# Performance work log

Hardware: AMD Instinct MI355X
Metric: run time of the kernel (lower is better)

The kernel has to match this reference:

```python
import jax, jax.numpy as jnp
import numpy as np

NPOINT = 2048
NSAMPLE = 32
BN_EPS = 1e-5


def fps(xyz_t, npoint):
    """Furthest point sampling. xyz_t: [B,N,3] -> idx [B,npoint] (starts at index 0)."""
    B, N, _ = xyz_t.shape

    def step(carry, _):
        dist, last = carry  # dist [B,N], last [B]
        centroid = jnp.take_along_axis(xyz_t, last[:, None, None], axis=1)  # [B,1,3]
        d = jnp.sum((xyz_t - centroid) ** 2, axis=-1)  # [B,N]
        dist = jnp.minimum(dist, d)
        nxt = jnp.argmax(dist, axis=1).astype(jnp.int32)
        return (dist, nxt), last

    init = (jnp.full((B, N), 1e10, xyz_t.dtype), jnp.zeros((B,), jnp.int32))
    _, idx = jax.lax.scan(step, init, None, length=npoint)  # [npoint,B]
    return jnp.transpose(idx)  # [B,npoint]


def knn(k, query_t, ref_t):
    """query_t [B,S,3], ref_t [B,N,3] -> k-nearest indices [B,S,k]."""
    d = (jnp.sum(query_t ** 2, -1)[:, :, None]
         + jnp.sum(ref_t ** 2, -1)[:, None, :]
         - 2.0 * jnp.einsum('bsc,bnc->bsn', query_t, ref_t))  # [B,S,N]
    _, idx = jax.lax.top_k(-d, k)
    return idx


def group(feat_t, idx):
    """feat_t [B,N,C], idx [B,S,K] -> [B,S,K,C] gathered neighbors."""
    return jax.vmap(lambda f, i: f[i])(feat_t, idx)


def setup_inputs():
    key = jax.random.key(0)
    ks = jax.random.split(key, 8)
    B, N, C, D = 8, 8192, 3, 3
    mlp = [32, 32, 64]
    inp = {
        'xyz': jax.random.normal(ks[0], (B, C, N), jnp.float32),
        'points': jax.random.normal(ks[1], (B, D, N), jnp.float32),
    }
    last = D + 3  # conv input channels = in_channel + 3
    for i, oc in enumerate(mlp):
        inp[f'w{i}'] = jax.random.normal(ks[2 + i], (oc, last), jnp.float32) * (1.0 / np.sqrt(last))
        inp[f'g{i}'] = jnp.ones((oc,), jnp.float32)
        inp[f'b{i}'] = jnp.zeros((oc,), jnp.float32)
        last = oc
    return inp


def reference(xyz, points, w0, g0, b0, w1, g1, b1, w2, g2, b2):
    xyz_t = jnp.transpose(xyz, (0, 2, 1))        # [B,N,3]
    points_t = jnp.transpose(points, (0, 2, 1))  # [B,N,D]

    fps_idx = fps(xyz_t, NPOINT)                             # [B,S]
    new_xyz_t = jax.vmap(lambda f, i: f[i])(xyz_t, fps_idx)  # [B,S,3]

    knn_idx = knn(NSAMPLE, new_xyz_t, xyz_t)                 # [B,S,K]
    grouped_xyz = group(xyz_t, knn_idx)                      # [B,S,K,3]
    pos_diff = grouped_xyz - new_xyz_t[:, :, None, :]        # [B,S,K,3]
    grouped_pts = group(points_t, knn_idx)                   # [B,S,K,D]

    x = jnp.concatenate([pos_diff, grouped_pts], axis=-1)    # [B,S,K,3+D]
    for w, g, b in ((w0, g0, b0), (w1, g1, b1), (w2, g2, b2)):
        x = jnp.einsum('oc,bskc->bsko', w, x)                # 1x1 conv, no bias
        mean = jnp.mean(x, axis=(0, 1, 2))                   # BatchNorm2d (training stats)
        var = jnp.var(x, axis=(0, 1, 2))
        x = jax.nn.relu(g * (x - mean) * jax.lax.rsqrt(var + BN_EPS) + b)

    new_points = jnp.max(x, axis=2)  # max over K neighbors -> [B,S,C']
    new_xyz = jnp.transpose(new_xyz_t, (0, 2, 1))      # [B,3,S]
    new_points = jnp.transpose(new_points, (0, 2, 1))  # [B,C',S]
    return (new_xyz, new_points, fps_idx)
```

## Files before the change

kernel.cpp:

```cpp
#include <hip/hip_runtime.h>
#include <hip/hip_bf16.h>
#include <math.h>


#define NB 8
#define NN 8192
#define NS 2048
#define NK 32

__global__ __launch_bounds__(256) void prep_kernel(const float* __restrict__ xyz,
                                                   const float* __restrict__ pts,
                                                   float4* __restrict__ xyz4,
                                                   float4* __restrict__ pts4,
                                                   float* __restrict__ stats_acc,
                                                   int* __restrict__ prog) {
  int tid = threadIdx.x;
  if (blockIdx.x == 0) {
    stats_acc[tid] = 0.f;
    if (tid < 8) prog[tid] = 0;
  }
  int g = blockIdx.x * 256 + tid;
  int b = g >> 13, n = g & 8191;
  const float* xb = xyz + b * 3 * NN;
  float x = xb[n], y = xb[NN + n], z = xb[2 * NN + n];
  xyz4[g] = make_float4(x, y, z, fmaf(x, x, fmaf(y, y, z * z)));
  const float* pb = pts + b * 3 * NN;
  pts4[g] = make_float4(pb[n], pb[NN + n], pb[2 * NN + n], 0.f);
}

template <int CTRL>
__device__ __forceinline__ float dpp_max(float v) {
  int o = __builtin_amdgcn_update_dpp(__float_as_int(v), __float_as_int(v),
                                      CTRL, 0xf, 0xf, false);
  return fmaxf(v, __int_as_float(o));
}

__device__ __forceinline__ void insert32(float (&a)[32], float f) {
#pragma unroll
  for (int i = 31; i >= 1; --i) a[i] = fminf(a[i], fmaxf(a[i - 1], f));
  a[0] = fminf(a[0], f);
}

union MegaShm {
  struct {
    float lxyz[3 * NN];
    unsigned long long wslot[2][8];
  } f;
  float lbuf[256][33];
};

__global__ __launch_bounds__(512, 1) void mega_kernel(
    const float4* __restrict__ xyz4, const float4* __restrict__ pts4,
    float4* __restrict__ nxyz4, int* __restrict__ knn,
    const float* __restrict__ w0, float* __restrict__ stats_acc,
    int* __restrict__ prog, float* __restrict__ out_nxyz,
    float* __restrict__ out_fps) {
  __shared__ MegaShm sh;
  int tid = threadIdx.x;
  int lane = tid & 63, wid = tid >> 6;

  if (blockIdx.x < 8) {
    int b = blockIdx.x;
    const float4* xb = xyz4 + b * NN;

    for (int i = tid; i < NN; i += 512) {
      float4 t = xb[i];
      sh.f.lxyz[3 * i] = t.x;
      sh.f.lxyz[3 * i + 1] = t.y;
      sh.f.lxyz[3 * i + 2] = t.z;
    }
    float ax[16], ay[16], az[16], dist[16];
#pragma unroll
    for (int j = 0; j < 16; ++j) {
      float4 t = xb[(tid << 4) + j];
      asm volatile("v_accvgpr_write_b32 %0, %1" : "=a"(ax[j]) : "v"(t.x));
      asm volatile("v_accvgpr_write_b32 %0, %1" : "=a"(ay[j]) : "v"(t.y));
      asm volatile("v_accvgpr_write_b32 %0, %1" : "=a"(az[j]) : "v"(t.z));
      dist[j] = 1e10f;
    }
    float4 c0 = xb[0];
    float cx = c0.x, cy = c0.y, cz = c0.z;
    if (tid == 0) {
      nxyz4[b * NS] = c0;
      out_nxyz[b * 3 * NS] = c0.x;
      out_nxyz[b * 3 * NS + NS] = c0.y;
      out_nxyz[b * 3 * NS + 2 * NS] = c0.z;
      out_fps[b * NS] = 0.f;
    }
    __syncthreads();

    for (int s = 1; s < NS; ++s) {
#pragma unroll
      for (int j = 0; j < 16; ++j) {
        float x, y, z;
        asm volatile("v_accvgpr_read_b32 %0, %1" : "=v"(x) : "a"(ax[j]));
        asm volatile("v_accvgpr_read_b32 %0, %1" : "=v"(y) : "a"(ay[j]));
        asm volatile("v_accvgpr_read_b32 %0, %1" : "=v"(z) : "a"(az[j]));
        float dx = __fsub_rn(x, cx);
        float dy = __fsub_rn(y, cy);
        float dz = __fsub_rn(z, cz);
        float d = __fadd_rn(__fadd_rn(__fmul_rn(dx, dx), __fmul_rn(dy, dy)),
                            __fmul_rn(dz, dz));
        dist[j] = fminf(dist[j], d);
      }
      float lmax = dist[0];
#pragma unroll
      for (int j = 1; j < 16; ++j) lmax = fmaxf(lmax, dist[j]);

      float m = lmax;
      m = dpp_max<0x111>(m);
      m = dpp_max<0x112>(m);
      m = dpp_max<0x114>(m);
      m = dpp_max<0x118>(m);
      m = dpp_max<0x142>(m);
      m = dpp_max<0x143>(m);
      float wmax = __int_as_float(__builtin_amdgcn_readlane(__float_as_int(m), 63));

      unsigned long long bl = __ballot(lmax == wmax);
      int l0 = __ffsll(bl) - 1;
      int bj = 0;
      if (lmax == wmax) {
#pragma unroll
        for (int t = 15; t >= 0; --t)
          if (dist[t] == lmax) bj = t;
      }
      int gcand = (tid << 4) + bj;
      int gw = __builtin_amdgcn_readlane(gcand, l0);

      if (lane == 0)
        sh.f.wslot[s & 1][wid] =
            (((unsigned long long)__float_as_uint(wmax)) << 32) |
            (unsigned)(8191 - gw);
      __syncthreads();

      unsigned long long vm = sh.f.wslot[s & 1][0];
#pragma unroll
      for (int k = 1; k < 8; ++k) {
        unsigned long long o = sh.f.wslot[s & 1][k];
        vm = o > vm ? o : vm;
      }
      int gid = 8191 - (int)(unsigned)(vm & 0xFFFFFFFFull);
      gid = __builtin_amdgcn_readfirstlane(gid);

      cx = sh.f.lxyz[3 * gid];
      cy = sh.f.lxyz[3 * gid + 1];
      cz = sh.f.lxyz[3 * gid + 2];
      if (tid == 0) {
        float w = fmaf(cx, cx, fmaf(cy, cy, cz * cz));
        nxyz4[b * NS + s] = make_float4(cx, cy, cz, w);
        out_nxyz[b * 3 * NS + s] = cx;
        out_nxyz[b * 3 * NS + NS + s] = cy;
        out_nxyz[b * 3 * NS + 2 * NS + s] = cz;
        out_fps[b * NS + s] = (float)gid;
        if (((s + 1) & 63) == 0) {
          __threadfence();
          __hip_atomic_store(&prog[b], s + 1, __ATOMIC_RELEASE,
                             __HIP_MEMORY_SCOPE_AGENT);
        }
      }
    }
    return;
  }

  int w = blockIdx.x - 8;
  for (int ti = 0; ti < 2; ++ti) {
    if (ti == 1 && w >= 8) break;
    int tile_id = (ti == 0) ? w : 248 + w;
    int b = tile_id >> 5, tile = tile_id & 31;
    const float4* xb = xyz4 + b * NN;
    const float4* pb = pts4 + b * NN;

    if (tid == 0) {
      int need = (tile + 1) * 64;
      while (__hip_atomic_load(&prog[b], __ATOMIC_ACQUIRE,
                               __HIP_MEMORY_SCOPE_AGENT) < need)
        __builtin_amdgcn_s_sleep(64);
    }
    __syncthreads();

    float arr[32];
    if (tid < 256) {
      int q = tid & 63, chunk = tid >> 6;
      float4 Q = nxyz4[b * NS + tile * 64 + q];
      float qq = Q.w;
      float mx = -2.f * Q.x, my = -2.f * Q.y, mz = -2.f * Q.z;
#pragma unroll
      for (int i = 0; i < 32; ++i) arr[i] = __uint_as_float(0x7f7fffffu);
      const float4* refs = xb + chunk * 2048;
      int rbase = chunk * 2048;
      for (int r = 0; r < 2048; r += 4) {
        float4 R0 = refs[r], R1 = refs[r + 1], R2 = refs[r + 2], R3 = refs[r + 3];
        float d0 = fmaxf(fmaf(R0.x, mx, fmaf(R0.y, my, fmaf(R0.z, mz, R0.w + qq))), 0.f);
        float d1 = fmaxf(fmaf(R1.x, mx, fmaf(R1.y, my, fmaf(R1.z, mz, R1.w + qq))), 0.f);
        float d2 = fmaxf(fmaf(R2.x, mx, fmaf(R2.y, my, fmaf(R2.z, mz, R2.w + qq))), 0.f);
        float d3 = fmaxf(fmaf(R3.x, mx, fmaf(R3.y, my, fmaf(R3.z, mz, R3.w + qq))), 0.f);
        float f0 = __uint_as_float((__float_as_uint(d0) & 0xFFFFE000u) | (unsigned)(rbase + r));
        float f1 = __uint_as_float((__float_as_uint(d1) & 0xFFFFE000u) | (unsigned)(rbase + r + 1));
        float f2 = __uint_as_float((__float_as_uint(d2) & 0xFFFFE000u) | (unsigned)(rbase + r + 2));
        float f3 = __uint_as_float((__float_as_uint(d3) & 0xFFFFE000u) | (unsigned)(rbase + r + 3));
        if (f0 < arr[31]) insert32(arr, f0);
        if (f1 < arr[31]) insert32(arr, f1);
        if (f2 < arr[31]) insert32(arr, f2);
        if (f3 < arr[31]) insert32(arr, f3);
      }
#pragma unroll
      for (int i = 0; i < 32; ++i) sh.lbuf[tid][i] = arr[i];
    }
    __syncthreads();
    if (tid < 64) {
      for (int c = 1; c < 4; ++c)
        for (int i = 0; i < 32; ++i) {
          float f = sh.lbuf[c * 64 + tid][i];
          if (f < arr[31]) insert32(arr, f);
        }
      int base = (b * NS + tile * 64 + tid) * NK;
#pragma unroll
      for (int i = 0; i < 32; ++i) {
        knn[base + i] = (int)(__float_as_uint(arr[i]) & 0x1FFFu);
        sh.lbuf[tid][i] = arr[i];
      }
    }
    __syncthreads();

    float sum[32], sumsq[32];
#pragma unroll
    for (int o = 0; o < 32; ++o) { sum[o] = 0.f; sumsq[o] = 0.f; }
    for (int t = 0; t < 4; ++t) {
      int e = tid * 4 + t;
      int sq = e >> 5, k = e & 31;
      int nid = (int)(__float_as_uint(sh.lbuf[sq][k]) & 0x1FFFu);
      float4 Q = nxyz4[b * NS + tile * 64 + sq];
      float4 R = xb[nid];
      float4 P = pb[nid];
      float x0[6] = {R.x - Q.x, R.y - Q.y, R.z - Q.z, P.x, P.y, P.z};
#pragma unroll
      for (int o = 0; o < 32; ++o) {
        float a = w0[o * 6] * x0[0];
#pragma unroll
        for (int c = 1; c < 6; ++c) a = fmaf(w0[o * 6 + c], x0[c], a);
        sum[o] += a;
        sumsq[o] = fmaf(a, a, sumsq[o]);
      }
    }
#pragma unroll
    for (int o = 0; o < 32; ++o) {
      float s = sum[o], q = sumsq[o];
#pragma unroll
      for (int d = 1; d < 64; d <<= 1) { s += __shfl_xor(s, d); q += __shfl_xor(q, d); }
      sum[o] = s; sumsq[o] = q;
    }
    __syncthreads();
    float* cmb = &sh.lbuf[0][0];
    if (lane == 0) {
#pragma unroll
      for (int o = 0; o < 32; ++o) {
        cmb[wid * 64 + o] = sum[o];
        cmb[wid * 64 + 32 + o] = sumsq[o];
      }
    }
    __syncthreads();
    if (tid < 64) {
      float tot = 0.f;
#pragma unroll
      for (int wv = 0; wv < 8; ++wv) tot += cmb[wv * 64 + tid];
      atomicAdd(&stats_acc[tid], tot);
    }
    __syncthreads();
  }
}

template <int STAGE>
__global__ __launch_bounds__(256) void mlp_kernel(
    const float4* __restrict__ xyz4, const float4* __restrict__ pts4,
    const float4* __restrict__ nxyz4, const int* __restrict__ knn,
    const float* __restrict__ w0, const float* __restrict__ w1,
    const float* __restrict__ w2, const float* __restrict__ ab,
    float* __restrict__ acc, float* __restrict__ out_np) {
  constexpr int C = (STAGE == 2) ? 64 : 32;
  constexpr int SM = (STAGE == 3) ? 8 * 64 * 32 : 512;
  __shared__ float smem[SM];
  int blk = blockIdx.x;
  int b = blk >> 6, s0 = (blk & 63) * 32;
  int tid = threadIdx.x, sl = tid & 31, ksec = tid >> 5;
  int lane = tid & 63, wid = tid >> 6;
  int s = s0 + sl;
  float4 Q = nxyz4[b * NS + s];
  const float4* xb = xyz4 + b * NN;
  const float4* pb = pts4 + b * NN;
  const int* kb = knn + (b * NS + s) * NK + ksec * 4;

  float acc1[(STAGE == 3) ? 64 : C];
  float acc2[(STAGE == 3) ? 1 : C];
  if constexpr (STAGE == 3) {
#pragma unroll
    for (int o = 0; o < 64; ++o) acc1[o] = -3.4e38f;
  } else {
#pragma unroll
    for (int o = 0; o < C; ++o) { acc1[o] = 0.f; acc2[o] = 0.f; }
  }

  for (int kk = 0; kk < 4; ++kk) {
    int nid = kb[kk];
    float4 R = xb[nid];
    float4 P = pb[nid];
    float x0[6] = {R.x - Q.x, R.y - Q.y, R.z - Q.z, P.x, P.y, P.z};
    float h[32];
#pragma unroll
    for (int o = 0; o < 32; ++o) {
      float a = w0[o * 6] * x0[0];
#pragma unroll
      for (int c = 1; c < 6; ++c) a = fmaf(w0[o * 6 + c], x0[c], a);
      h[o] = fmaxf(fmaf(a, ab[o], ab[64 + o]), 0.f);
    }
    float h1[32];
#pragma unroll
    for (int o = 0; o < 32; ++o) {
      float a = 0.f;
#pragma unroll
      for (int i = 0; i < 32; ++i) a = fmaf(w1[o * 32 + i], h[i], a);
      h1[o] = a;
    }
    if constexpr (STAGE == 1) {
#pragma unroll
      for (int o = 0; o < 32; ++o) { acc1[o] += h1[o]; acc2[o] = fmaf(h1[o], h1[o], acc2[o]); }
    } else {
#pragma unroll
      for (int o = 0; o < 32; ++o) h1[o] = fmaxf(fmaf(h1[o], ab[128 + o], ab[192 + o]), 0.f);
#pragma unroll
      for (int o = 0; o < 64; ++o) {
        float a = 0.f;
#pragma unroll
        for (int i = 0; i < 32; ++i) a = fmaf(w2[o * 32 + i], h1[i], a);
        if constexpr (STAGE == 2) {
          acc1[o] += a;
          acc2[o] = fmaf(a, a, acc2[o]);
        } else {
          acc1[o] = fmaxf(acc1[o], fmaxf(fmaf(a, ab[256 + o], ab[320 + o]), 0.f));
        }
      }
    }
  }

  if constexpr (STAGE < 3) {
#pragma unroll
    for (int o = 0; o < C; ++o) {
      float v1 = acc1[o], v2 = acc2[o];
#pragma unroll
      for (int d = 1; d < 64; d <<= 1) { v1 += __shfl_xor(v1, d); v2 += __shfl_xor(v2, d); }
      acc1[o] = v1; acc2[o] = v2;
    }
    if (lane == 0) {
#pragma unroll
      for (int o = 0; o < C; ++o) {
        smem[wid * 2 * C + o] = acc1[o];
        smem[wid * 2 * C + C + o] = acc2[o];
      }
    }
    __syncthreads();
    if (tid < 2 * C) {
      float v = smem[tid] + smem[2 * C + tid] + smem[4 * C + tid] + smem[6 * C + tid];
      atomicAdd(&acc[tid], v);
    }
  } else {
#pragma unroll
    for (int o = 0; o < 64; ++o) smem[ksec * 2048 + o * 32 + sl] = acc1[o];
    __syncthreads();
#pragma unroll
    for (int i = 0; i < 8; ++i) {
      int e = i * 256 + tid;
      int ch = e >> 5, ss = e & 31;
      float v = smem[ch * 32 + ss];
#pragma unroll
      for (int ks = 1; ks < 8; ++ks) v = fmaxf(v, smem[ks * 2048 + ch * 32 + ss]);
      out_np[b * 64 * NS + ch * NS + s0 + ss] = v;
    }
  }
}

__global__ __launch_bounds__(64) void finalize_kernel(const float* __restrict__ acc,
                                                      const float* __restrict__ g,
                                                      const float* __restrict__ bt,
                                                      float* __restrict__ ab, int C) {
  int tid = threadIdx.x;
  if (tid < C) {
    float s1 = acc[tid];
    float s2 = acc[C + tid];
    const float ninv = 1.0f / 524288.0f;
    float mean = s1 * ninv;
    float var = s2 * ninv - mean * mean;
    float inv = 1.0f / sqrtf(var + 1e-5f);
    float a = g[tid] * inv;
    ab[tid] = a;
    ab[64 + tid] = bt[tid] - mean * a;
  }
}

extern "C" void kernel_launch(void* const* d_in, const int* in_sizes, int n_in,
                              void* d_out, int out_size, void* d_ws, size_t ws_size,
                              hipStream_t stream) {
  const float* xyz = (const float*)d_in[0];
  const float* pts = (const float*)d_in[1];
  const float* w0 = (const float*)d_in[2];
  const float* g0 = (const float*)d_in[3];
  const float* b0 = (const float*)d_in[4];
  const float* w1 = (const float*)d_in[5];
  const float* g1 = (const float*)d_in[6];
  const float* b1 = (const float*)d_in[7];
  const float* w2 = (const float*)d_in[8];
  const float* g2 = (const float*)d_in[9];
  const float* b2 = (const float*)d_in[10];
  float* out = (float*)d_out;
  float* ws = (float*)d_ws;

  float4* xyz4 = (float4*)ws;
  float4* pts4 = (float4*)(ws + 262144);
  float4* nxyz4 = (float4*)(ws + 524288);
  int* knn = (int*)(ws + 589824);
  float* stats_acc = ws + 1114112;
  int* prog = (int*)(ws + 1114368);
  float* ab = ws + 1114432;
  float* out_np = out + 49152;
  float* out_fps = out + 1097728;

  prep_kernel<<<256, 256, 0, stream>>>(xyz, pts, xyz4, pts4, stats_acc, prog);
  mega_kernel<<<256, 512, 0, stream>>>(xyz4, pts4, nxyz4, knn, w0, stats_acc,
                                       prog, out, out_fps);
  finalize_kernel<<<1, 64, 0, stream>>>(stats_acc, g0, b0, ab, 32);
  mlp_kernel<1><<<512, 256, 0, stream>>>(xyz4, pts4, nxyz4, knn, w0, w1, w2, ab,
                                         stats_acc + 64, nullptr);
  finalize_kernel<<<1, 64, 0, stream>>>(stats_acc + 64, g1, b1, ab + 128, 32);
  mlp_kernel<2><<<512, 256, 0, stream>>>(xyz4, pts4, nxyz4, knn, w0, w1, w2, ab,
                                         stats_acc + 128, nullptr);
  finalize_kernel<<<1, 64, 0, stream>>>(stats_acc + 128, g2, b2, ab + 256, 64);
  mlp_kernel<3><<<512, 256, 0, stream>>>(xyz4, pts4, nxyz4, knn, w0, w1, w2, ab,
                                         nullptr, out_np);
}
```

Measured before the change: 3.241 ms.

## Use packed FP32 math in FPS loop and batch centroid output writes

The furthest-point-sampling distance update now processes two points per instruction using v_pk_add_f32/v_pk_mul_f32, halving VALU instruction count in the serial loop. Per-step global stores of the selected centroid are replaced by a shared-memory ring of 64 entries, flushed cooperatively by 64 threads every 64 steps before the progress flag is published. This removes store latency from each serial iteration at the cost of two extra block barriers per 64 steps.

```diff
diff --git a/kernel.cpp b/kernel.cpp
--- a/kernel.cpp
+++ b/kernel.cpp
@@ -7,6 +7,15 @@
 #define NN 8192
 #define NS 2048
 #define NK 32
+
+typedef float v2f __attribute__((ext_vector_type(2)));
+
+__device__ __forceinline__ v2f pk_add(v2f a, v2f b) {
+  v2f d; asm("v_pk_add_f32 %0, %1, %2" : "=v"(d) : "v"(a), "v"(b)); return d;
+}
+__device__ __forceinline__ v2f pk_mul(v2f a, v2f b) {
+  v2f d; asm("v_pk_mul_f32 %0, %1, %2" : "=v"(d) : "v"(a), "v"(b)); return d;
+}
 
 __global__ __launch_bounds__(256) void prep_kernel(const float* __restrict__ xyz,
                                                    const float* __restrict__ pts,
@@ -45,6 +54,7 @@
   struct {
     float lxyz[3 * NN];
     unsigned long long wslot[2][8];
+    float4 cbuf[64];
   } f;
   float lbuf[256][33];
 };
@@ -80,28 +90,28 @@
     }
     float4 c0 = xb[0];
     float cx = c0.x, cy = c0.y, cz = c0.z;
-    if (tid == 0) {
-      nxyz4[b * NS] = c0;
-      out_nxyz[b * 3 * NS] = c0.x;
-      out_nxyz[b * 3 * NS + NS] = c0.y;
-      out_nxyz[b * 3 * NS + 2 * NS] = c0.z;
-      out_fps[b * NS] = 0.f;
-    }
+    if (tid == 0)
+      sh.f.cbuf[0] = make_float4(c0.x, c0.y, c0.z, 0.f);
     __syncthreads();
 
     for (int s = 1; s < NS; ++s) {
-#pragma unroll
-      for (int j = 0; j < 16; ++j) {
-        float x, y, z;
-        asm volatile("v_accvgpr_read_b32 %0, %1" : "=v"(x) : "a"(ax[j]));
-        asm volatile("v_accvgpr_read_b32 %0, %1" : "=v"(y) : "a"(ay[j]));
-        asm volatile("v_accvgpr_read_b32 %0, %1" : "=v"(z) : "a"(az[j]));
-        float dx = __fsub_rn(x, cx);
-        float dy = __fsub_rn(y, cy);
-        float dz = __fsub_rn(z, cz);
-        float d = __fadd_rn(__fadd_rn(__fmul_rn(dx, dx), __fmul_rn(dy, dy)),
-                            __fmul_rn(dz, dz));
-        dist[j] = fminf(dist[j], d);
+      v2f ncx = {-cx, -cx}, ncy = {-cy, -cy}, ncz = {-cz, -cz};
+#pragma unroll
+      for (int k = 0; k < 8; ++k) {
+        float x0, x1, y0, y1, z0, z1;
+        asm volatile("v_accvgpr_read_b32 %0, %1" : "=v"(x0) : "a"(ax[2 * k]));
+        asm volatile("v_accvgpr_read_b32 %0, %1" : "=v"(x1) : "a"(ax[2 * k + 1]));
+        asm volatile("v_accvgpr_read_b32 %0, %1" : "=v"(y0) : "a"(ay[2 * k]));
+        asm volatile("v_accvgpr_read_b32 %0, %1" : "=v"(y1) : "a"(ay[2 * k + 1]));
+        asm volatile("v_accvgpr_read_b32 %0, %1" : "=v"(z0) : "a"(az[2 * k]));
+        asm volatile("v_accvgpr_read_b32 %0, %1" : "=v"(z1) : "a"(az[2 * k + 1]));
+        v2f x01 = {x0, x1}, y01 = {y0, y1}, z01 = {z0, z1};
+        v2f dx = pk_add(x01, ncx);
+        v2f dy = pk_add(y01, ncy);
+        v2f dz = pk_add(z01, ncz);
+        v2f ss = pk_add(pk_add(pk_mul(dx, dx), pk_mul(dy, dy)), pk_mul(dz, dz));
+        dist[2 * k] = fminf(dist[2 * k], ss.x);
+        dist[2 * k + 1] = fminf(dist[2 * k + 1], ss.y);
       }
       float lmax = dist[0];
 #pragma unroll
@@ -145,14 +155,23 @@
       cx = sh.f.lxyz[3 * gid];
       cy = sh.f.lxyz[3 * gid + 1];
       cz = sh.f.lxyz[3 * gid + 2];
-      if (tid == 0) {
-        float w = fmaf(cx, cx, fmaf(cy, cy, cz * cz));
-        nxyz4[b * NS + s] = make_float4(cx, cy, cz, w);
-        out_nxyz[b * 3 * NS + s] = cx;
-        out_nxyz[b * 3 * NS + NS + s] = cy;
-        out_nxyz[b * 3 * NS + 2 * NS + s] = cz;
-        out_fps[b * NS + s] = (float)gid;
-        if (((s + 1) & 63) == 0) {
+      if (tid == 0)
+        sh.f.cbuf[s & 63] = make_float4(cx, cy, cz, (float)gid);
+
+      if (((s + 1) & 63) == 0) {
+        __syncthreads();
+        if (tid < 64) {
+          int sp = (s & ~63) + tid;
+          float4 cc = sh.f.cbuf[tid];
+          float w = fmaf(cc.x, cc.x, fmaf(cc.y, cc.y, cc.z * cc.z));
+          nxyz4[b * NS + sp] = make_float4(cc.x, cc.y, cc.z, w);
+          out_nxyz[b * 3 * NS + sp] = cc.x;
+          out_nxyz[b * 3 * NS + NS + sp] = cc.y;
+          out_nxyz[b * 3 * NS + 2 * NS + sp] = cc.z;
+          out_fps[b * NS + sp] = cc.w;
+        }
+        __syncthreads();
+        if (tid == 0) {
           __threadfence();
           __hip_atomic_store(&prog[b], s + 1, __ATOMIC_RELEASE,
                              __HIP_MEMORY_SCOPE_AGENT);
```

New measurement: 3.440 ms. +6.2%, slower.
